# Optimization experiments

Measured on AMD Instinct MI355X. Metric: run time of the kernel, lower is better.

The kernel has to match this reference:

```python
import jax, jax.numpy as jnp
import numpy as np

B = 4096
T = 66            # total_char_ids = 51 + 8 + 6 + 1
EMB = 128
ITEM_EMB = 64     # emb_dim // 2
NUM_ITEMS = 287
ITEMS_IN_GAME = 70  # 7 * 10
N_SCREEN = 24
N_MINI = 40
CONT = 32


def _unique_ids(key, batch, n):
    keys = jax.random.split(key, batch)
    return jax.vmap(lambda k: jax.random.permutation(k, T)[:n])(keys).astype(jnp.int32)


def setup_inputs() -> dict:
    key = jax.random.key(0)
    ks = jax.random.split(key, 16)
    inp = {
        "continuous_f": jax.random.normal(ks[0], (B, CONT), jnp.float32),
        "screen_feats": jax.random.uniform(ks[1], (B, N_SCREEN, 4), jnp.float32),
        "minimap_feats": jax.random.uniform(ks[2], (B, N_MINI, 2), jnp.float32),
        "char_emb": jax.random.normal(ks[3], (T, EMB), jnp.float32) * 0.02,
        "item_emb": jax.random.normal(ks[4], (NUM_ITEMS, ITEM_EMB), jnp.float32) * 0.02,
        "Ws1": jax.random.normal(ks[5], (EMB + 4, EMB), jnp.float32) * 0.05,
        "bs1": jnp.zeros((EMB,), jnp.float32),
        "Ws2": jax.random.normal(ks[6], (EMB, EMB), jnp.float32) * 0.05,
        "bs2": jnp.zeros((EMB,), jnp.float32),
        "Wm1": jax.random.normal(ks[7], (EMB + 2, EMB), jnp.float32) * 0.05,
        "bm1": jnp.zeros((EMB,), jnp.float32),
        "Wm2": jax.random.normal(ks[8], (EMB, EMB), jnp.float32) * 0.05,
        "bm2": jnp.zeros((EMB,), jnp.float32),
        "screen_ids": _unique_ids(ks[9], B, N_SCREEN),
        "minimap_ids": _unique_ids(ks[10], B, N_MINI),
        "items": jax.random.randint(ks[11], (B, ITEMS_IN_GAME), 0, NUM_ITEMS, jnp.int32),
    }
    return inp


def reference(continuous_f, screen_feats, minimap_feats, char_emb, item_emb,
              Ws1, bs1, Ws2, bs2, Wm1, bm1, Wm2, bm2,
              screen_ids, minimap_ids, items):
    b = continuous_f.shape[0]
    rows = jnp.arange(b)[:, None]

    # scatter detections by char id into fixed [T, .] buffers (vectorized over batch)
    scr = jnp.zeros((b, T, 4), screen_feats.dtype).at[rows, screen_ids].set(screen_feats)
    mini = jnp.zeros((b, T, 2), minimap_feats.dtype).at[rows, minimap_ids].set(minimap_feats)

    # item embedding lookup -> [b, 70*64]
    item_flat = item_emb[items].reshape(b, -1)

    base = jnp.broadcast_to(char_emb, (b, T, EMB))  # all char ids embedded

    def mlp(x, W1, b1, W2, b2):
        h = jax.nn.relu(jnp.einsum('btf,fh->bth', x, W1) + b1)
        return jnp.einsum('bth,hk->btk', h, W2) + b2

    screen_out = mlp(jnp.concatenate([base, scr], axis=-1), Ws1, bs1, Ws2, bs2)
    mini_out = mlp(jnp.concatenate([base, mini], axis=-1), Wm1, bm1, Wm2, bm2)

    obs = jnp.concatenate(
        [continuous_f, screen_out.reshape(b, -1), mini_out.reshape(b, -1), item_flat],
        axis=-1)  # [b, 32 + 66*128 + 66*128 + 70*64] = [b, 21408]
    return obs
```

## Files before the change

### kernel.cpp

```cpp
#include <hip/hip_runtime.h>
#include <stdint.h>

#define BDIM 512
#define PDIM 512
#define T_   66
#define EMB  128
#define NS   24
#define NM   40
#define NI   70
#define CONT 32
#define OUTW 21408

typedef __attribute__((ext_vector_type(4))) float f32x4;
typedef __attribute__((ext_vector_type(8))) unsigned short u16x8;
typedef __attribute__((ext_vector_type(8))) __bf16 bf16x8;

static __device__ __forceinline__ unsigned short f2bf(float x) {
  union { float f; unsigned u; } v; v.f = x;
  unsigned r = (v.u + 0x7FFFu + ((v.u >> 16) & 1u)) >> 16;
  return (unsigned short)r;
}

static __device__ __forceinline__ f32x4 mfma16(u16x8 a, u16x8 b, f32x4 c) {
  return __builtin_amdgcn_mfma_f32_16x16x32_bf16(
      __builtin_bit_cast(bf16x8, a), __builtin_bit_cast(bf16x8, b), c, 0, 0, 0);
}

__global__ __launch_bounds__(PDIM) void precomp(
    const float* __restrict__ char_emb,
    const float* __restrict__ Ws1, const float* __restrict__ bs1,
    const float* __restrict__ Ws2, const float* __restrict__ bs2,
    const float* __restrict__ Wm1, const float* __restrict__ bm1,
    const float* __restrict__ Wm2, const float* __restrict__ bm2,
    float* __restrict__ base_h_s, float* __restrict__ base_h_m,
    float* __restrict__ base_out_s, float* __restrict__ base_out_m,
    unsigned short* __restrict__ w2s_swz, unsigned short* __restrict__ w2m_swz) {
  const int bb = blockIdx.x, tid = threadIdx.x;
  if (bb < T_) {
    const int t = bb;
    const int quarter = tid >> 7;
    const int col = tid & 127;
    const int mlp = quarter & 1;
    const int kh = quarter >> 1;
    const float* W1 = mlp ? Wm1 : Ws1;
    const float* W2 = mlp ? Wm2 : Ws2;
    const float* b1 = mlp ? bm1 : bs1;
    const float* b2 = mlp ? bm2 : bs2;
    float* bh = mlp ? base_h_m : base_h_s;
    float* bo = mlp ? base_out_m : base_out_s;
    __shared__ float part[4][EMB];
    __shared__ float h[2][EMB];
    float acc = 0.f;
#pragma unroll 8
    for (int f = kh * 64; f < kh * 64 + 64; ++f)
      acc += char_emb[t * EMB + f] * W1[f * EMB + col];
    part[quarter][col] = acc;
    __syncthreads();
    if (tid < 256) {
      const float v = b1[col] + part[mlp][col] + part[2 + mlp][col];
      bh[t * EMB + col] = v;
      h[mlp][col] = fmaxf(v, 0.f);
    }
    __syncthreads();
    float acc2 = 0.f;
#pragma unroll 8
    for (int i = kh * 64; i < kh * 64 + 64; ++i)
      acc2 += h[mlp][i] * W2[i * EMB + col];
    part[quarter][col] = acc2;
    __syncthreads();
    if (tid < 256)
      bo[t * EMB + col] = b2[col] + part[mlp][col] + part[2 + mlp][col];
  } else {
    const int mlp = bb - T_;
    const float* W2 = mlp ? Wm2 : Ws2;
    unsigned short* dst = mlp ? w2m_swz : w2s_swz;
    for (int idx = tid; idx < 8 * 4 * 64 * 8; idx += PDIM) {
      const int e = idx & 7, lane = (idx >> 3) & 63, kk = (idx >> 9) & 3, n = idx >> 11;
      const int k = kk * 32 + (lane >> 4) * 8 + e;
      const int col = n * 16 + (lane & 15);
      dst[idx] = f2bf(W2[k * EMB + col]);
    }
  }
}

__global__ __launch_bounds__(BDIM) void fused(
    const float* __restrict__ contf,
    const float* __restrict__ sfeat,
    const float* __restrict__ mfeat,
    const float* __restrict__ item_emb,
    const float* __restrict__ Ws1,
    const float* __restrict__ bs2,
    const float* __restrict__ Wm1,
    const float* __restrict__ bm2,
    const int* __restrict__ sids,
    const int* __restrict__ mids,
    const int* __restrict__ items,
    const float* __restrict__ base_h_s, const float* __restrict__ base_h_m,
    const float* __restrict__ base_out_s, const float* __restrict__ base_out_m,
    const unsigned short* __restrict__ w2s_swz, const unsigned short* __restrict__ w2m_swz,
    float* __restrict__ out) {
  const int b = blockIdx.x, tid = threadIdx.x;

  __shared__ int s_map[T_], m_map[T_];
  __shared__ int s_id[NS], m_id[NM], s_item[NI];
  __shared__ float s_f[NS * 4], m_f[NM * 2];
  __shared__ u16x8 h_frag[5 * 4 * 64];

  if (tid < T_) { s_map[tid] = -1; m_map[tid] = -1; }
  if (tid < NS) s_id[tid] = sids[b * NS + tid];
  if (tid < NM) m_id[tid] = mids[b * NM + tid];
  if (tid < NI) s_item[tid] = items[b * NI + tid];
  if (tid < NS * 4) s_f[tid] = sfeat[b * NS * 4 + tid];
  if (tid < NM * 2) m_f[tid] = mfeat[b * NM * 2 + tid];
  __syncthreads();

  if (tid < NS) s_map[s_id[tid]] = tid;
  if (tid < NM) m_map[m_id[tid]] = tid;
  for (int u = tid; u < 5 * 4 * 64; u += BDIM) {
    const int lane = u & 63, kk = (u >> 6) & 3, tile = u >> 8;
    const int g = lane >> 4, r = lane & 15;
    const int k0 = kk * 32 + g * 8;
    const bool scr = tile < 2;
    const int j = scr ? tile * 16 + r : (tile - 2) * 16 + r;
    const int nd = scr ? NS : NM;
    float v[8];
    if (j < nd) {
      const int t = scr ? s_id[j] : m_id[j];
      const float* bh = (scr ? base_h_s : base_h_m) + t * EMB + k0;
#pragma unroll
      for (int e = 0; e < 8; ++e) v[e] = bh[e];
      if (scr) {
        const float* fp = &s_f[j * 4];
#pragma unroll
        for (int c = 0; c < 4; ++c) {
          const float fc = fp[c];
          const float* wp = Ws1 + (128 + c) * EMB + k0;
#pragma unroll
          for (int e = 0; e < 8; ++e) v[e] += fc * wp[e];
        }
      } else {
        const float* fp = &m_f[j * 2];
#pragma unroll
        for (int c = 0; c < 2; ++c) {
          const float fc = fp[c];
          const float* wp = Wm1 + (128 + c) * EMB + k0;
#pragma unroll
          for (int e = 0; e < 8; ++e) v[e] += fc * wp[e];
        }
      }
#pragma unroll
      for (int e = 0; e < 8; ++e) v[e] = fmaxf(v[e], 0.f);
    } else {
#pragma unroll
      for (int e = 0; e < 8; ++e) v[e] = 0.f;
    }
    u16x8 pk;
#pragma unroll
    for (int e = 0; e < 8; ++e) pk[e] = f2bf(v[e]);
    h_frag[u] = pk;
  }
  __syncthreads();

  const int lane = tid & 63, w = tid >> 6;
  const int g = lane >> 4, r = lane & 15;
  const int n = w;
  float* outS = out + (size_t)b * OUTW + CONT;
  float* outM = outS + T_ * EMB;

  u16x8 bS[4], bM[4];
#pragma unroll
  for (int kk = 0; kk < 4; ++kk) {
    bS[kk] = reinterpret_cast<const u16x8*>(w2s_swz)[(n * 4 + kk) * 64 + lane];
    bM[kk] = reinterpret_cast<const u16x8*>(w2m_swz)[(n * 4 + kk) * 64 + lane];
  }
  const float biasS = bs2[n * 16 + r];
  const float biasM = bm2[n * 16 + r];

#pragma unroll
  for (int m = 0; m < 2; ++m) {
    f32x4 acc = {biasS, biasS, biasS, biasS};
#pragma unroll
    for (int kk = 0; kk < 4; ++kk)
      acc = mfma16(h_frag[(m * 4 + kk) * 64 + lane], bS[kk], acc);
#pragma unroll
    for (int q = 0; q < 4; ++q) {
      const int rd = m * 16 + g * 4 + q;
      if (rd < NS) {
        const int t = s_id[rd];
        __builtin_nontemporal_store(acc[q], outS + t * EMB + n * 16 + r);
      }
    }
  }
#pragma unroll
  for (int m = 0; m < 3; ++m) {
    f32x4 acc = {biasM, biasM, biasM, biasM};
#pragma unroll
    for (int kk = 0; kk < 4; ++kk)
      acc = mfma16(h_frag[((m + 2) * 4 + kk) * 64 + lane], bM[kk], acc);
#pragma unroll
    for (int q = 0; q < 4; ++q) {
      const int rd = m * 16 + g * 4 + q;
      if (rd < NM) {
        const int t = m_id[rd];
        __builtin_nontemporal_store(acc[q], outM + t * EMB + n * 16 + r);
      }
    }
  }

  for (int u = tid; u < T_ * 32; u += BDIM) {
    const int t = u >> 5, q = u & 31;
    if (s_map[t] < 0) {
      const f32x4 v = reinterpret_cast<const f32x4*>(base_out_s + t * EMB)[q];
      __builtin_nontemporal_store(v, reinterpret_cast<f32x4*>(outS + t * EMB) + q);
    }
  }
  for (int u = tid; u < T_ * 32; u += BDIM) {
    const int t = u >> 5, q = u & 31;
    if (m_map[t] < 0) {
      const f32x4 v = reinterpret_cast<const f32x4*>(base_out_m + t * EMB)[q];
      __builtin_nontemporal_store(v, reinterpret_cast<f32x4*>(outM + t * EMB) + q);
    }
  }

  {
    f32x4* ob = reinterpret_cast<f32x4*>(out + (size_t)b * OUTW);
    const f32x4* cb = reinterpret_cast<const f32x4*>(contf + (size_t)b * CONT);
    float* outI = out + (size_t)b * OUTW + (CONT + 2 * T_ * EMB);
    for (int u = tid; u < 8 + NI * 16; u += BDIM) {
      if (u < 8) {
        __builtin_nontemporal_store(cb[u], &ob[u]);
      } else {
        const int v2 = u - 8, j = v2 >> 4, q = v2 & 15;
        const int it = s_item[j];
        const f32x4 src = reinterpret_cast<const f32x4*>(item_emb + it * 64)[q];
        __builtin_nontemporal_store(src, reinterpret_cast<f32x4*>(outI + j * 64) + q);
      }
    }
  }
}

extern "C" void kernel_launch(void* const* d_in, const int* in_sizes, int n_in,
                              void* d_out, int out_size, void* d_ws, size_t ws_size,
                              hipStream_t stream) {
  const float* contf    = (const float*)d_in[0];
  const float* sfeat    = (const float*)d_in[1];
  const float* mfeat    = (const float*)d_in[2];
  const float* char_emb = (const float*)d_in[3];
  const float* item_emb = (const float*)d_in[4];
  const float* Ws1 = (const float*)d_in[5];
  const float* bs1 = (const float*)d_in[6];
  const float* Ws2 = (const float*)d_in[7];
  const float* bs2 = (const float*)d_in[8];
  const float* Wm1 = (const float*)d_in[9];
  const float* bm1 = (const float*)d_in[10];
  const float* Wm2 = (const float*)d_in[11];
  const float* bm2 = (const float*)d_in[12];
  const int* sids  = (const int*)d_in[13];
  const int* mids  = (const int*)d_in[14];
  const int* items = (const int*)d_in[15];
  float* out = (float*)d_out;

  const int B = in_sizes[0] / CONT;

  char* ws = (char*)d_ws;
  float* base_h_s   = (float*)(ws + 0);
  float* base_h_m   = (float*)(ws + 33792);
  float* base_out_s = (float*)(ws + 67584);
  float* base_out_m = (float*)(ws + 101376);
  unsigned short* w2s = (unsigned short*)(ws + 135168);
  unsigned short* w2m = (unsigned short*)(ws + 167936);

  precomp<<<T_ + 2, PDIM, 0, stream>>>(char_emb, Ws1, bs1, Ws2, bs2, Wm1, bm1, Wm2, bm2,
                                       base_h_s, base_h_m, base_out_s, base_out_m, w2s, w2m);
  fused<<<B, BDIM, 0, stream>>>(contf, sfeat, mfeat, item_emb, Ws1, bs2, Wm1, bm2,
                                sids, mids, items,
                                base_h_s, base_h_m, base_out_s, base_out_m, w2s, w2m, out);
}
```

Before: 99.00 us.

## Split each sample across two specialized blocks: MFMA compute vs copy

The fused kernel now launches two 256-thread blocks per sample. Odd blocks compute the detected-row MLP outputs with MFMA, each wave covering two column tiles. Even blocks copy the precomputed base rows for undetected ids, the continuous features and the item embeddings, using a compacted list of undetected ids instead of a per-row branch. The aim is better occupancy and overlap of compute-heavy and store-heavy work. The list sizes are hardcoded (42 and 26), which is only correct because the ids per sample are unique.

```diff
diff --git a/kernel.cpp b/kernel.cpp
--- a/kernel.cpp
+++ b/kernel.cpp
@@ -1,12 +1,14 @@
 #include <hip/hip_runtime.h>
 #include <stdint.h>
 
-#define BDIM 512
+#define BDIM 256
 #define PDIM 512
 #define T_   66
 #define EMB  128
 #define NS   24
 #define NM   40
+#define NBS  42
+#define NBM  26
 #define NI   70
 #define CONT 32
 #define OUTW 21408
@@ -83,7 +85,7 @@
   }
 }
 
-__global__ __launch_bounds__(BDIM) void fused(
+__global__ __launch_bounds__(BDIM, 5) void fused(
     const float* __restrict__ contf,
     const float* __restrict__ sfeat,
     const float* __restrict__ mfeat,
@@ -99,142 +101,163 @@
     const float* __restrict__ base_out_s, const float* __restrict__ base_out_m,
     const unsigned short* __restrict__ w2s_swz, const unsigned short* __restrict__ w2m_swz,
     float* __restrict__ out) {
-  const int b = blockIdx.x, tid = threadIdx.x;
-
-  __shared__ int s_map[T_], m_map[T_];
-  __shared__ int s_id[NS], m_id[NM], s_item[NI];
+  const int bid = blockIdx.x, tid = threadIdx.x;
+  const int b = bid >> 1;
+
+  __shared__ int s_id[NS], m_id[NM];
   __shared__ float s_f[NS * 4], m_f[NM * 2];
   __shared__ u16x8 h_frag[5 * 4 * 64];
-
-  if (tid < T_) { s_map[tid] = -1; m_map[tid] = -1; }
-  if (tid < NS) s_id[tid] = sids[b * NS + tid];
-  if (tid < NM) m_id[tid] = mids[b * NM + tid];
-  if (tid < NI) s_item[tid] = items[b * NI + tid];
-  if (tid < NS * 4) s_f[tid] = sfeat[b * NS * 4 + tid];
-  if (tid < NM * 2) m_f[tid] = mfeat[b * NM * 2 + tid];
-  __syncthreads();
-
-  if (tid < NS) s_map[s_id[tid]] = tid;
-  if (tid < NM) m_map[m_id[tid]] = tid;
-  for (int u = tid; u < 5 * 4 * 64; u += BDIM) {
-    const int lane = u & 63, kk = (u >> 6) & 3, tile = u >> 8;
+  __shared__ int s_map[T_], m_map[T_];
+  __shared__ int listS[T_], listM[T_], s_item[NI];
+  __shared__ int cntS, cntM;
+
+  float* outS = out + (size_t)b * OUTW + CONT;
+  float* outM = outS + T_ * EMB;
+
+  if (bid & 1) {
+    if (tid < NS) s_id[tid] = sids[b * NS + tid];
+    if (tid < NM) m_id[tid] = mids[b * NM + tid];
+    if (tid < NS * 4) s_f[tid] = sfeat[b * NS * 4 + tid];
+    if (tid < NM * 2) m_f[tid] = mfeat[b * NM * 2 + tid];
+    __syncthreads();
+
+    for (int u = tid; u < 5 * 4 * 64; u += BDIM) {
+      const int lane = u & 63, kk = (u >> 6) & 3, tile = u >> 8;
+      const int g = lane >> 4, r = lane & 15;
+      const int k0 = kk * 32 + g * 8;
+      const bool scr = tile < 2;
+      const int j = scr ? tile * 16 + r : (tile - 2) * 16 + r;
+      const int nd = scr ? NS : NM;
+      float v[8];
+      if (j < nd) {
+        const int t = scr ? s_id[j] : m_id[j];
+        const float* bh = (scr ? base_h_s : base_h_m) + t * EMB + k0;
+#pragma unroll
+        for (int e = 0; e < 8; ++e) v[e] = bh[e];
+        if (scr) {
+          const float* fp = &s_f[j * 4];
+#pragma unroll
+          for (int c = 0; c < 4; ++c) {
+            const float fc = fp[c];
+            const float* wp = Ws1 + (128 + c) * EMB + k0;
+#pragma unroll
+            for (int e = 0; e < 8; ++e) v[e] += fc * wp[e];
+          }
+        } else {
+          const float* fp = &m_f[j * 2];
+#pragma unroll
+          for (int c = 0; c < 2; ++c) {
+            const float fc = fp[c];
+            const float* wp = Wm1 + (128 + c) * EMB + k0;
+#pragma unroll
+            for (int e = 0; e < 8; ++e) v[e] += fc * wp[e];
+          }
+        }
+#pragma unroll
+        for (int e = 0; e < 8; ++e) v[e] = fmaxf(v[e], 0.f);
+      } else {
+#pragma unroll
+        for (int e = 0; e < 8; ++e) v[e] = 0.f;
+      }
+      u16x8 pk;
+#pragma unroll
+      for (int e = 0; e < 8; ++e) pk[e] = f2bf(v[e]);
+      h_frag[u] = pk;
+    }
+    __syncthreads();
+
+    const int lane = tid & 63, w = tid >> 6;
     const int g = lane >> 4, r = lane & 15;
-    const int k0 = kk * 32 + g * 8;
-    const bool scr = tile < 2;
-    const int j = scr ? tile * 16 + r : (tile - 2) * 16 + r;
-    const int nd = scr ? NS : NM;
-    float v[8];
-    if (j < nd) {
-      const int t = scr ? s_id[j] : m_id[j];
-      const float* bh = (scr ? base_h_s : base_h_m) + t * EMB + k0;
-#pragma unroll
-      for (int e = 0; e < 8; ++e) v[e] = bh[e];
-      if (scr) {
-        const float* fp = &s_f[j * 4];
-#pragma unroll
-        for (int c = 0; c < 4; ++c) {
-          const float fc = fp[c];
-          const float* wp = Ws1 + (128 + c) * EMB + k0;
-#pragma unroll
-          for (int e = 0; e < 8; ++e) v[e] += fc * wp[e];
-        }
-      } else {
-        const float* fp = &m_f[j * 2];
-#pragma unroll
-        for (int c = 0; c < 2; ++c) {
-          const float fc = fp[c];
-          const float* wp = Wm1 + (128 + c) * EMB + k0;
-#pragma unroll
-          for (int e = 0; e < 8; ++e) v[e] += fc * wp[e];
+    const int n0 = w * 2;
+
+    u16x8 bb[2][4];
+    float bias[2];
+#pragma unroll
+    for (int n = 0; n < 2; ++n) {
+      bias[n] = bs2[(n0 + n) * 16 + r];
+#pragma unroll
+      for (int kk = 0; kk < 4; ++kk)
+        bb[n][kk] = reinterpret_cast<const u16x8*>(w2s_swz)[((n0 + n) * 4 + kk) * 64 + lane];
+    }
+#pragma unroll
+    for (int m = 0; m < 2; ++m) {
+#pragma unroll
+      for (int n = 0; n < 2; ++n) {
+        f32x4 acc = {bias[n], bias[n], bias[n], bias[n]};
+#pragma unroll
+        for (int kk = 0; kk < 4; ++kk)
+          acc = mfma16(h_frag[(m * 4 + kk) * 64 + lane], bb[n][kk], acc);
+#pragma unroll
+        for (int q = 0; q < 4; ++q) {
+          const int rd = m * 16 + g * 4 + q;
+          if (rd < NS) {
+            const int t = s_id[rd];
+            __builtin_nontemporal_store(acc[q], outS + t * EMB + (n0 + n) * 16 + r);
+          }
         }
       }
-#pragma unroll
-      for (int e = 0; e < 8; ++e) v[e] = fmaxf(v[e], 0.f);
-    } else {
-#pragma unroll
-      for (int e = 0; e < 8; ++e) v[e] = 0.f;
-    }
-    u16x8 pk;
-#pragma unroll
-    for (int e = 0; e < 8; ++e) pk[e] = f2bf(v[e]);
-    h_frag[u] = pk;
-  }
-  __syncthreads();
-
-  const int lane = tid & 63, w = tid >> 6;
-  const int g = lane >> 4, r = lane & 15;
-  const int n = w;
-  float* outS = out + (size_t)b * OUTW + CONT;
-  float* outM = outS + T_ * EMB;
-
-  u16x8 bS[4], bM[4];
-#pragma unroll
-  for (int kk = 0; kk < 4; ++kk) {
-    bS[kk] = reinterpret_cast<const u16x8*>(w2s_swz)[(n * 4 + kk) * 64 + lane];
-    bM[kk] = reinterpret_cast<const u16x8*>(w2m_swz)[(n * 4 + kk) * 64 + lane];
-  }
-  const float biasS = bs2[n * 16 + r];
-  const float biasM = bm2[n * 16 + r];
-
-#pragma unroll
-  for (int m = 0; m < 2; ++m) {
-    f32x4 acc = {biasS, biasS, biasS, biasS};
-#pragma unroll
-    for (int kk = 0; kk < 4; ++kk)
-      acc = mfma16(h_frag[(m * 4 + kk) * 64 + lane], bS[kk], acc);
-#pragma unroll
-    for (int q = 0; q < 4; ++q) {
-      const int rd = m * 16 + g * 4 + q;
-      if (rd < NS) {
-        const int t = s_id[rd];
-        __builtin_nontemporal_store(acc[q], outS + t * EMB + n * 16 + r);
+    }
+#pragma unroll
+    for (int n = 0; n < 2; ++n) {
+      bias[n] = bm2[(n0 + n) * 16 + r];
+#pragma unroll
+      for (int kk = 0; kk < 4; ++kk)
+        bb[n][kk] = reinterpret_cast<const u16x8*>(w2m_swz)[((n0 + n) * 4 + kk) * 64 + lane];
+    }
+#pragma unroll
+    for (int m = 0; m < 3; ++m) {
+#pragma unroll
+      for (int n = 0; n < 2; ++n) {
+        f32x4 acc = {bias[n], bias[n], bias[n], bias[n]};
+#pragma unroll
+        for (int kk = 0; kk < 4; ++kk)
+          acc = mfma16(h_frag[((m + 2) * 4 + kk) * 64 + lane], bb[n][kk], acc);
+#pragma unroll
+        for (int q = 0; q < 4; ++q) {
+          const int rd = m * 16 + g * 4 + q;
+          if (rd < NM) {
+            const int t = m_id[rd];
+            __builtin_nontemporal_store(acc[q], outM + t * EMB + (n0 + n) * 16 + r);
+          }
+        }
       }
     }
-  }
-#pragma unroll
-  for (int m = 0; m < 3; ++m) {
-    f32x4 acc = {biasM, biasM, biasM, biasM};
-#pragma unroll
-    for (int kk = 0; kk < 4; ++kk)
-      acc = mfma16(h_frag[((m + 2) * 4 + kk) * 64 + lane], bM[kk], acc);
-#pragma unroll
-    for (int q = 0; q < 4; ++q) {
-      const int rd = m * 16 + g * 4 + q;
-      if (rd < NM) {
-        const int t = m_id[rd];
-        __builtin_nontemporal_store(acc[q], outM + t * EMB + n * 16 + r);
-      }
-    }
-  }
-
-  for (int u = tid; u < T_ * 32; u += BDIM) {
-    const int t = u >> 5, q = u & 31;
-    if (s_map[t] < 0) {
+  } else {
+    if (tid == 0) { cntS = 0; cntM = 0; }
+    if (tid < T_) { s_map[tid] = -1; m_map[tid] = -1; }
+    if (tid < NS) s_id[tid] = sids[b * NS + tid];
+    if (tid < NM) m_id[tid] = mids[b * NM + tid];
+    if (tid < NI) s_item[tid] = items[b * NI + tid];
+    __syncthreads();
+    if (tid < NS) s_map[s_id[tid]] = 1;
+    if (tid < NM) m_map[m_id[tid]] = 1;
+    __syncthreads();
+    if (tid < T_ && s_map[tid] < 0) { const int p = atomicAdd(&cntS, 1); listS[p] = tid; }
+    if (tid < T_ && m_map[tid] < 0) { const int p = atomicAdd(&cntM, 1); listM[p] = tid; }
+    __syncthreads();
+
+    if (tid < 8) {
+      const f32x4 v = reinterpret_cast<const f32x4*>(contf + (size_t)b * CONT)[tid];
+      __builtin_nontemporal_store(v, reinterpret_cast<f32x4*>(out + (size_t)b * OUTW) + tid);
+    }
+    for (int u = tid; u < NBS * 32; u += BDIM) {
+      const int d = u >> 5, q = u & 31;
+      const int t = listS[d];
       const f32x4 v = reinterpret_cast<const f32x4*>(base_out_s + t * EMB)[q];
       __builtin_nontemporal_store(v, reinterpret_cast<f32x4*>(outS + t * EMB) + q);
     }
-  }
-  for (int u = tid; u < T_ * 32; u += BDIM) {
-    const int t = u >> 5, q = u & 31;
-    if (m_map[t] < 0) {
+    for (int u = tid; u < NBM * 32; u += BDIM) {
+      const int d = u >> 5, q = u & 31;
+      const int t = listM[d];
       const f32x4 v = reinterpret_cast<const f32x4*>(base_out_m + t * EMB)[q];
       __builtin_nontemporal_store(v, reinterpret_cast<f32x4*>(outM + t * EMB) + q);
     }
-  }
-
-  {
-    f32x4* ob = reinterpret_cast<f32x4*>(out + (size_t)b * OUTW);
-    const f32x4* cb = reinterpret_cast<const f32x4*>(contf + (size_t)b * CONT);
     float* outI = out + (size_t)b * OUTW + (CONT + 2 * T_ * EMB);
-    for (int u = tid; u < 8 + NI * 16; u += BDIM) {
-      if (u < 8) {
-        __builtin_nontemporal_store(cb[u], &ob[u]);
-      } else {
-        const int v2 = u - 8, j = v2 >> 4, q = v2 & 15;
-        const int it = s_item[j];
-        const f32x4 src = reinterpret_cast<const f32x4*>(item_emb + it * 64)[q];
-        __builtin_nontemporal_store(src, reinterpret_cast<f32x4*>(outI + j * 64) + q);
-      }
+    for (int u = tid; u < NI * 16; u += BDIM) {
+      const int j = u >> 4, q = u & 15;
+      const int it = s_item[j];
+      const f32x4 v = reinterpret_cast<const f32x4*>(item_emb + it * 64)[q];
+      __builtin_nontemporal_store(v, reinterpret_cast<f32x4*>(outI + j * 64) + q);
     }
   }
 }
@@ -272,7 +295,7 @@
 
   precomp<<<T_ + 2, PDIM, 0, stream>>>(char_emb, Ws1, bs1, Ws2, bs2, Wm1, bm1, Wm2, bm2,
                                        base_h_s, base_h_m, base_out_s, base_out_m, w2s, w2m);
-  fused<<<B, BDIM, 0, stream>>>(contf, sfeat, mfeat, item_emb, Ws1, bs2, Wm1, bm2,
-                                sids, mids, items,
-                                base_h_s, base_h_m, base_out_s, base_out_m, w2s, w2m, out);
-}
+  fused<<<2 * B, BDIM, 0, stream>>>(contf, sfeat, mfeat, item_emb, Ws1, bs2, Wm1, bm2,
+                                    sids, mids, items,
+                                    base_h_s, base_h_m, base_out_s, base_out_m, w2s, w2m, out);
+}
```

After: 122.4 us. +23.7%, slower.
